# Kernel tuning notes

Hardware: AMD Instinct MI355X
Metric: run time of the kernel (lower is better)

Reference implementation:

```python
import jax, jax.numpy as jnp
import numpy as np

# Material constants (from init_kwargs: E=1e4, nu=0.3)
E_MOD = 1.0e4
NU = 0.3
MU = E_MOD / (2.0 * (1.0 + NU))                      # shear modulus
LMBDA = E_MOD * NU / ((1.0 + NU) * (1.0 - 2.0 * NU))  # first Lame parameter
EPS = 1e-10

B, N_NODES, N_ELEM, N_QUAD, NPE = 4, 100000, 500000, 4, 4  # tet4 mesh


def setup_inputs() -> dict:
    key = jax.random.key(0)
    k1, k2, k3, k4 = jax.random.split(key, 4)
    # small displacements so J = det(I + grad_u) stays positive
    u = jax.random.normal(k1, (B, N_NODES, 3), dtype=jnp.float32) * 0.01
    elements = jax.random.randint(k2, (N_ELEM, NPE), 0, N_NODES)
    # precomputed shape-function derivatives dN/dx per element/quad point
    dN_dx = jax.random.normal(k3, (N_ELEM, N_QUAD, NPE, 3), dtype=jnp.float32) * 0.1
    # positive Jacobian determinants of the reference->physical map
    detJ = jax.random.uniform(k4, (N_ELEM, N_QUAD), dtype=jnp.float32, minval=0.5, maxval=1.5) * 1e-3
    # tet4 4-point quadrature weights: 0.25 / 6
    quad_weights = jnp.full((N_QUAD,), 0.25 / 6.0, dtype=jnp.float32)
    return {"u": u, "elements": elements, "dN_dx": dN_dx, "detJ": detJ,
            "quad_weights": quad_weights}


def reference(u, elements, dN_dx, detJ, quad_weights):
    # gather nodal displacements per element: [B, E, n, 3]
    elem_u = u[:, elements]
    # grad_u[b,e,q,i,j] = sum_n elem_u[b,e,n,i] * dN_dx[e,q,n,j]  -> [B,E,Q,3,3]
    grad_u = jnp.einsum('beni,eqnj->beqij', elem_u, dN_dx)
    F = grad_u + jnp.eye(3, dtype=u.dtype)
    J = jnp.linalg.det(F)                      # [B,E,Q]
    I_C = jnp.sum(F * F, axis=(-2, -1))        # tr(F^T F)
    logJ = jnp.log(jnp.maximum(J, EPS))
    W = 0.5 * MU * (I_C - 3.0 - 2.0 * logJ) + 0.25 * LMBDA * (J * J - 1.0 - 2.0 * logJ)
    # quadrature-weighted assembly over elements and quad points -> [B]
    return jnp.einsum('beq,eq,q->b', W, detJ, quad_weights)
```

## Files before the change

### kernel.cpp

```cpp
#include <hip/hip_runtime.h>

#define MU_C   3846.1538461538462f
#define LM_C   5769.2307692307695f
#define LOGC   (MU_C + 0.5f * LM_C)
#define EPS_C  1e-10f

#define NBLK 1024

__global__ __launch_bounds__(256) void nh_transpose_u_pad(
    const float* __restrict__ u, float4* __restrict__ ut, int n_nodes)
{
    const int i = blockIdx.x * 256 + threadIdx.x;
    if (i >= n_nodes) return;
    float4* q = ut + (size_t)i * 4;
    #pragma unroll
    for (int b = 0; b < 4; ++b) {
        const float* p = u + ((size_t)b * n_nodes + i) * 3;
        q[b] = make_float4(p[0], p[1], p[2], 0.f);
    }
}

__device__ __forceinline__ float nh_energy(
    const float4* dn,
    const float4* uu,
    const float*  wqv)
{
    const float* d  = reinterpret_cast<const float*>(dn);
    const float* us = reinterpret_cast<const float*>(uu);
    float a = 0.f;
    #pragma unroll
    for (int q = 0; q < 4; ++q) {
        float F[3][3];
        #pragma unroll
        for (int i = 0; i < 3; ++i) {
            #pragma unroll
            for (int j = 0; j < 3; ++j) {
                float g = 0.f;
                #pragma unroll
                for (int n = 0; n < 4; ++n)
                    g = fmaf(us[n * 4 + i], d[(q*4 + n)*3 + j], g);
                F[i][j] = g + ((i == j) ? 1.f : 0.f);
            }
        }
        const float J =
              F[0][0] * (F[1][1]*F[2][2] - F[1][2]*F[2][1])
            - F[0][1] * (F[1][0]*F[2][2] - F[1][2]*F[2][0])
            + F[0][2] * (F[1][0]*F[2][1] - F[1][1]*F[2][0]);
        float IC = 0.f;
        #pragma unroll
        for (int i = 0; i < 3; ++i)
            #pragma unroll
            for (int j = 0; j < 3; ++j)
                IC = fmaf(F[i][j], F[i][j], IC);
        const float lj = __logf(fmaxf(J, EPS_C));
        const float W = 0.5f * MU_C * (IC - 3.f)
                      + 0.25f * LM_C * fmaf(J, J, -1.f)
                      - LOGC * lj;
        a = fmaf(W, wqv[q], a);
    }
    return a;
}

__global__ __launch_bounds__(256) void nh_partial_v10(
    const float4* __restrict__ ut,
    const int4*   __restrict__ elp,
    const float4* __restrict__ dnp,
    const float4* __restrict__ djp,
    const float*  __restrict__ qw,
    float* __restrict__ partial,
    int n_elem, int ntiles, int chunk)
{
    const int t = threadIdx.x;
    const int b = t & 3;
    const int p = t >> 2;
    const int t0  = blockIdx.x * chunk;
    const int cnt = min(chunk, ntiles - t0);

    __shared__ float s_red[4][4];

    float acc = 0.f;

    if (cnt > 0) {
        const float4 w4 = *reinterpret_cast<const float4*>(qw);
        const int nelmax = n_elem - 1;

        float4 dnA[12], dnB[12];
        float4 uuA[4],  uuB[4];
        float  wqA[4],  wqB[4];

        #define NH_LOAD(DN, UU, WQ, M)                                        \
        {                                                                     \
            const int e  = (t0 + (M)) * 64 + p;                               \
            const int ec = min(e, nelmax);                                    \
            const int4   nd = elp[ec];                                        \
            const float4 dj = djp[ec];                                        \
            const float4* dptr = dnp + (size_t)ec * 12;                       \
            _Pragma("unroll")                                                 \
            for (int k = 0; k < 12; ++k) DN[k] = dptr[k];                     \
            UU[0] = ut[nd.x * 4 + b];                                         \
            UU[1] = ut[nd.y * 4 + b];                                         \
            UU[2] = ut[nd.z * 4 + b];                                         \
            UU[3] = ut[nd.w * 4 + b];                                         \
            const float vs = (e < n_elem) ? 1.f : 0.f;                        \
            WQ[0] = dj.x * w4.x * vs; WQ[1] = dj.y * w4.y * vs;               \
            WQ[2] = dj.z * w4.z * vs; WQ[3] = dj.w * w4.w * vs;               \
        }

        NH_LOAD(dnA, uuA, wqA, 0)
        if (cnt > 1) NH_LOAD(dnB, uuB, wqB, 1)

        for (int m = 0; m < cnt; m += 2) {
            acc += nh_energy(dnA, uuA, wqA);
            if (m + 2 < cnt) NH_LOAD(dnA, uuA, wqA, m + 2)
            if (m + 1 < cnt) acc += nh_energy(dnB, uuB, wqB);
            if (m + 3 < cnt) NH_LOAD(dnB, uuB, wqB, m + 3)
        }
        #undef NH_LOAD
    }

    #pragma unroll
    for (int off = 32; off >= 4; off >>= 1)
        acc += __shfl_down(acc, off);

    const int lane = t & 63;
    const int wid  = t >> 6;
    if (lane < 4) s_red[wid][lane] = acc;
    __syncthreads();
    if (t < 4)
        partial[(size_t)blockIdx.x * 4 + t] =
            (s_red[0][t] + s_red[1][t]) + (s_red[2][t] + s_red[3][t]);
}

__global__ __launch_bounds__(256) void nh_final(
    const float* __restrict__ partial,
    float* __restrict__ out,
    int nparts)
{
    float accb[4] = {0.f, 0.f, 0.f, 0.f};
    for (int i = threadIdx.x; i < nparts; i += 256) {
        const float4 p = reinterpret_cast<const float4*>(partial)[i];
        accb[0] += p.x; accb[1] += p.y; accb[2] += p.z; accb[3] += p.w;
    }

    #pragma unroll
    for (int b = 0; b < 4; ++b) {
        float v = accb[b];
        #pragma unroll
        for (int off = 32; off > 0; off >>= 1)
            v += __shfl_down(v, off);
        accb[b] = v;
    }

    __shared__ float lds[4][4];
    const int lane = threadIdx.x & 63;
    const int wid  = threadIdx.x >> 6;
    if (lane == 0) {
        #pragma unroll
        for (int b = 0; b < 4; ++b) lds[wid][b] = accb[b];
    }
    __syncthreads();
    if (threadIdx.x == 0) {
        #pragma unroll
        for (int b = 0; b < 4; ++b)
            out[b] = (lds[0][b] + lds[1][b]) + (lds[2][b] + lds[3][b]);
    }
}

extern "C" void kernel_launch(void* const* d_in, const int* in_sizes, int n_in,
                              void* d_out, int out_size, void* d_ws, size_t ws_size,
                              hipStream_t stream) {
    const float* u        = (const float*)d_in[0];
    const int*   elements = (const int*)d_in[1];
    const float* dN_dx    = (const float*)d_in[2];
    const float* detJ     = (const float*)d_in[3];
    const float* qw       = (const float*)d_in[4];
    float* out = (float*)d_out;

    const int B       = out_size;
    const int n_nodes = in_sizes[0] / (3 * B);
    const int n_elem  = in_sizes[1] / 4;

    const int threads = 256;
    const int ntiles  = (n_elem + 63) / 64;
    const int nblocks = (ntiles < NBLK) ? ntiles : NBLK;
    const int chunk   = (ntiles + nblocks - 1) / nblocks;

    const size_t ut_bytes = (size_t)n_nodes * 4 * sizeof(float4);
    float4* ut     = (float4*)d_ws;
    float* partial = (float*)((char*)d_ws + ut_bytes);

    const int tb = (n_nodes + threads - 1) / threads;
    nh_transpose_u_pad<<<tb, threads, 0, stream>>>(u, ut, n_nodes);

    nh_partial_v10<<<nblocks, threads, 0, stream>>>(
        ut, reinterpret_cast<const int4*>(elements),
        reinterpret_cast<const float4*>(dN_dx),
        reinterpret_cast<const float4*>(detJ),
        qw, partial, n_elem, ntiles, chunk);

    nh_final<<<1, threads, 0, stream>>>(partial, out, nblocks);
}
```

Baseline: 58.24 us.

## Stage dN_dx, connectivity and detJ tiles through double-buffered LDS with coalesced nontemporal loads

Replaces per-thread strided register loads of each element's 48 dN_dx floats with coalesced block-wide float4 loads into a double-buffered shared-memory slab, padded to 52 floats per element. Connectivity and detJ are also staged in LDS, and the next tile is prefetched while the current one is computed. Streaming data uses nontemporal loads so it does not pollute the cache used by the gathered displacements. In exchange it adds two barriers per tile, uses about 30KB of LDS per block, and reads dN_dx from LDS, which may limit occupancy.

```diff
diff --git a/kernel.cpp b/kernel.cpp
--- a/kernel.cpp
+++ b/kernel.cpp
@@ -5,6 +5,11 @@
 #define LOGC   (MU_C + 0.5f * LM_C)
 #define EPS_C  1e-10f
 
+typedef float nf4 __attribute__((ext_vector_type(4)));
+typedef int   ni4 __attribute__((ext_vector_type(4)));
+
+#define ELB  64
+#define SLAB 52
 #define NBLK 1024
 
 __global__ __launch_bounds__(256) void nh_transpose_u_pad(
@@ -20,16 +25,23 @@
     }
 }
 
-__device__ __forceinline__ float nh_energy(
-    const float4* dn,
-    const float4* uu,
-    const float*  wqv)
-{
-    const float* d  = reinterpret_cast<const float*>(dn);
-    const float* us = reinterpret_cast<const float*>(uu);
+__device__ __forceinline__ float nh_energy_slab(
+    const float* slab, const float4* uu, const float* wq)
+{
+    float eu[4][3];
+    eu[0][0]=uu[0].x; eu[0][1]=uu[0].y; eu[0][2]=uu[0].z;
+    eu[1][0]=uu[1].x; eu[1][1]=uu[1].y; eu[1][2]=uu[1].z;
+    eu[2][0]=uu[2].x; eu[2][1]=uu[2].y; eu[2][2]=uu[2].z;
+    eu[3][0]=uu[3].x; eu[3][1]=uu[3].y; eu[3][2]=uu[3].z;
+
     float a = 0.f;
     #pragma unroll
     for (int q = 0; q < 4; ++q) {
+        const float4 f0 = *reinterpret_cast<const float4*>(slab + q*12 + 0);
+        const float4 f1 = *reinterpret_cast<const float4*>(slab + q*12 + 4);
+        const float4 f2 = *reinterpret_cast<const float4*>(slab + q*12 + 8);
+        const float d[12] = {f0.x,f0.y,f0.z,f0.w, f1.x,f1.y,f1.z,f1.w,
+                             f2.x,f2.y,f2.z,f2.w};
         float F[3][3];
         #pragma unroll
         for (int i = 0; i < 3; ++i) {
@@ -38,7 +50,7 @@
                 float g = 0.f;
                 #pragma unroll
                 for (int n = 0; n < 4; ++n)
-                    g = fmaf(us[n * 4 + i], d[(q*4 + n)*3 + j], g);
+                    g = fmaf(eu[n][i], d[n*3 + j], g);
                 F[i][j] = g + ((i == j) ? 1.f : 0.f);
             }
         }
@@ -56,66 +68,107 @@
         const float W = 0.5f * MU_C * (IC - 3.f)
                       + 0.25f * LM_C * fmaf(J, J, -1.f)
                       - LOGC * lj;
-        a = fmaf(W, wqv[q], a);
+        a = fmaf(W, wq[q], a);
     }
     return a;
 }
 
-__global__ __launch_bounds__(256) void nh_partial_v10(
+__global__ __launch_bounds__(256) void nh_partial_v15(
     const float4* __restrict__ ut,
-    const int4*   __restrict__ elp,
-    const float4* __restrict__ dnp,
-    const float4* __restrict__ djp,
+    const ni4*    __restrict__ elp,
+    const nf4*    __restrict__ dnp,
+    const nf4*    __restrict__ djp,
     const float*  __restrict__ qw,
     float* __restrict__ partial,
     int n_elem, int ntiles, int chunk)
 {
+    __shared__ float s_dn[2][ELB * SLAB];
+    __shared__ int   s_el[2][ELB * 4];
+    __shared__ float s_dj[2][ELB * 4];
+    __shared__ float s_red[4][4];
+
     const int t = threadIdx.x;
     const int b = t & 3;
     const int p = t >> 2;
+
     const int t0  = blockIdx.x * chunk;
     const int cnt = min(chunk, ntiles - t0);
 
-    __shared__ float s_red[4][4];
-
     float acc = 0.f;
 
     if (cnt > 0) {
         const float4 w4 = *reinterpret_cast<const float4*>(qw);
-        const int nelmax = n_elem - 1;
-
-        float4 dnA[12], dnB[12];
-        float4 uuA[4],  uuB[4];
-        float  wqA[4],  wqB[4];
-
-        #define NH_LOAD(DN, UU, WQ, M)                                        \
-        {                                                                     \
-            const int e  = (t0 + (M)) * 64 + p;                               \
-            const int ec = min(e, nelmax);                                    \
-            const int4   nd = elp[ec];                                        \
-            const float4 dj = djp[ec];                                        \
-            const float4* dptr = dnp + (size_t)ec * 12;                       \
-            _Pragma("unroll")                                                 \
-            for (int k = 0; k < 12; ++k) DN[k] = dptr[k];                     \
-            UU[0] = ut[nd.x * 4 + b];                                         \
-            UU[1] = ut[nd.y * 4 + b];                                         \
-            UU[2] = ut[nd.z * 4 + b];                                         \
-            UU[3] = ut[nd.w * 4 + b];                                         \
-            const float vs = (e < n_elem) ? 1.f : 0.f;                        \
-            WQ[0] = dj.x * w4.x * vs; WQ[1] = dj.y * w4.y * vs;               \
-            WQ[2] = dj.z * w4.z * vs; WQ[3] = dj.w * w4.w * vs;               \
-        }
-
-        NH_LOAD(dnA, uuA, wqA, 0)
-        if (cnt > 1) NH_LOAD(dnB, uuB, wqB, 1)
-
-        for (int m = 0; m < cnt; m += 2) {
-            acc += nh_energy(dnA, uuA, wqA);
-            if (m + 2 < cnt) NH_LOAD(dnA, uuA, wqA, m + 2)
-            if (m + 1 < cnt) acc += nh_energy(dnB, uuB, wqB);
-            if (m + 3 < cnt) NH_LOAD(dnB, uuB, wqB, m + 3)
-        }
-        #undef NH_LOAD
+        const int dnmax = n_elem * 12 - 1;
+        const int elmax = n_elem - 1;
+        const int tlast = ntiles - 1;
+
+        const int oA = (t       / 12) * SLAB + (t       % 12) * 4;
+        const int oB = ((t+256) / 12) * SLAB + ((t+256) % 12) * 4;
+        const int oC = ((t+512) / 12) * SLAB + ((t+512) % 12) * 4;
+
+        float4 uuA[4], uuB[4];
+
+        {
+            const int base = t0 * 768;
+            const nf4 r0 = __builtin_nontemporal_load(dnp + min(base + t,       dnmax));
+            const nf4 r1 = __builtin_nontemporal_load(dnp + min(base + t + 256, dnmax));
+            const nf4 r2 = __builtin_nontemporal_load(dnp + min(base + t + 512, dnmax));
+            ni4 rel; nf4 rdj;
+            if (t < 64)       rel = __builtin_nontemporal_load(elp + min(t0*64 + t, elmax));
+            else if (t < 128) rdj = __builtin_nontemporal_load(djp + min(t0*64 + (t-64), elmax));
+            *reinterpret_cast<float4*>(&s_dn[0][oA]) = (const float4&)r0;
+            *reinterpret_cast<float4*>(&s_dn[0][oB]) = (const float4&)r1;
+            *reinterpret_cast<float4*>(&s_dn[0][oC]) = (const float4&)r2;
+            if (t < 64)       reinterpret_cast<int4*>(s_el[0])[t] = (const int4&)rel;
+            else if (t < 128) reinterpret_cast<float4*>(s_dj[0])[t-64] = (const float4&)rdj;
+            __syncthreads();
+            const int4 nd = reinterpret_cast<const int4*>(s_el[0])[p];
+            uuA[0] = ut[(nd.x << 2) | b];
+            uuA[1] = ut[(nd.y << 2) | b];
+            uuA[2] = ut[(nd.z << 2) | b];
+            uuA[3] = ut[(nd.w << 2) | b];
+        }
+
+        #define NH_BODY(M, CUR, UUC, UUN)                                             \
+        {                                                                             \
+            const int tn = min(t0 + (M) + 1, tlast);                                  \
+            const int base = tn * 768;                                                \
+            const nf4 r0 = __builtin_nontemporal_load(dnp + min(base + t,       dnmax)); \
+            const nf4 r1 = __builtin_nontemporal_load(dnp + min(base + t + 256, dnmax)); \
+            const nf4 r2 = __builtin_nontemporal_load(dnp + min(base + t + 512, dnmax)); \
+            ni4 rel; nf4 rdj;                                                         \
+            if (t < 64)       rel = __builtin_nontemporal_load(elp + min(tn*64 + t, elmax)); \
+            else if (t < 128) rdj = __builtin_nontemporal_load(djp + min(tn*64 + (t-64), elmax)); \
+            {                                                                         \
+                const int e = (t0 + (M)) * 64 + p;                                    \
+                const float sc = ((M) < cnt && e < n_elem) ? 1.f : 0.f;               \
+                const float* dj4 = &s_dj[CUR][p * 4];                                 \
+                const float wq[4] = {dj4[0]*w4.x*sc, dj4[1]*w4.y*sc,                  \
+                                     dj4[2]*w4.z*sc, dj4[3]*w4.w*sc};                 \
+                acc += nh_energy_slab(&s_dn[CUR][p * SLAB], UUC, wq);                 \
+            }                                                                         \
+            __syncthreads();                                                          \
+            *reinterpret_cast<float4*>(&s_dn[(CUR)^1][oA]) = (const float4&)r0;       \
+            *reinterpret_cast<float4*>(&s_dn[(CUR)^1][oB]) = (const float4&)r1;       \
+            *reinterpret_cast<float4*>(&s_dn[(CUR)^1][oC]) = (const float4&)r2;       \
+            if (t < 64)       reinterpret_cast<int4*>(s_el[(CUR)^1])[t] = (const int4&)rel; \
+            else if (t < 128) reinterpret_cast<float4*>(s_dj[(CUR)^1])[t-64] = (const float4&)rdj; \
+            __syncthreads();                                                          \
+            {                                                                         \
+                const int4 nd = reinterpret_cast<const int4*>(s_el[(CUR)^1])[p];      \
+                UUN[0] = ut[(nd.x << 2) | b];                                         \
+                UUN[1] = ut[(nd.y << 2) | b];                                         \
+                UUN[2] = ut[(nd.z << 2) | b];                                         \
+                UUN[3] = ut[(nd.w << 2) | b];                                         \
+            }                                                                         \
+        }
+
+        const int iters = (cnt + 1) & ~1;
+        for (int m = 0; m < iters; m += 2) {
+            NH_BODY(m,     0, uuA, uuB)
+            NH_BODY(m + 1, 1, uuB, uuA)
+        }
+        #undef NH_BODY
     }
 
     #pragma unroll
@@ -132,16 +185,13 @@
 }
 
 __global__ __launch_bounds__(256) void nh_final(
-    const float* __restrict__ partial,
-    float* __restrict__ out,
-    int nparts)
+    const float* __restrict__ partial, float* __restrict__ out, int nparts)
 {
     float accb[4] = {0.f, 0.f, 0.f, 0.f};
     for (int i = threadIdx.x; i < nparts; i += 256) {
         const float4 p = reinterpret_cast<const float4*>(partial)[i];
         accb[0] += p.x; accb[1] += p.y; accb[2] += p.z; accb[3] += p.w;
     }
-
     #pragma unroll
     for (int b = 0; b < 4; ++b) {
         float v = accb[b];
@@ -150,7 +200,6 @@
             v += __shfl_down(v, off);
         accb[b] = v;
     }
-
     __shared__ float lds[4][4];
     const int lane = threadIdx.x & 63;
     const int wid  = threadIdx.x >> 6;
@@ -181,21 +230,21 @@
     const int n_elem  = in_sizes[1] / 4;
 
     const int threads = 256;
-    const int ntiles  = (n_elem + 63) / 64;
+    const int ntiles  = (n_elem + ELB - 1) / ELB;
     const int nblocks = (ntiles < NBLK) ? ntiles : NBLK;
     const int chunk   = (ntiles + nblocks - 1) / nblocks;
 
     const size_t ut_bytes = (size_t)n_nodes * 4 * sizeof(float4);
-    float4* ut     = (float4*)d_ws;
-    float* partial = (float*)((char*)d_ws + ut_bytes);
+    float4* ut      = (float4*)d_ws;
+    float*  partial = (float*)((char*)d_ws + ut_bytes);
 
     const int tb = (n_nodes + threads - 1) / threads;
     nh_transpose_u_pad<<<tb, threads, 0, stream>>>(u, ut, n_nodes);
 
-    nh_partial_v10<<<nblocks, threads, 0, stream>>>(
-        ut, reinterpret_cast<const int4*>(elements),
-        reinterpret_cast<const float4*>(dN_dx),
-        reinterpret_cast<const float4*>(detJ),
+    nh_partial_v15<<<nblocks, threads, 0, stream>>>(
+        ut, reinterpret_cast<const ni4*>(elements),
+        reinterpret_cast<const nf4*>(dN_dx),
+        reinterpret_cast<const nf4*>(detJ),
         qw, partial, n_elem, ntiles, chunk);
 
     nh_final<<<1, threads, 0, stream>>>(partial, out, nblocks);
```

After: 59.38 us. Within noise of the previous version (+2.0%).
